# Performance work log

Hardware: AMD Instinct MI355X
Metric: run time of the kernel (lower is better)

## Reference

```python
import jax, jax.numpy as jnp
import numpy as np
import math

B, S, E = 32, 4096, 1024
H, D = 16, 64          # n_head, model_dim (per-head qk dim)
NV = E // H            # per-head value dim

def setup_inputs() -> dict:
    key = jax.random.key(0)
    ks = jax.random.split(key, 8)
    sc = 1.0 / math.sqrt(E)
    return {
        "seq1": jax.random.normal(ks[0], (B, 1, E), jnp.float32),
        "seq2": jax.random.normal(ks[1], (B, S, E), jnp.float32),
        "mask": jax.random.randint(ks[2], (B, 1, 1, S), 0, 2, jnp.int32),
        "Wq": jax.random.normal(ks[3], (E, H * D), jnp.float32) * sc,
        "bq": jnp.zeros((H * D,), jnp.float32),
        "Wk": jax.random.normal(ks[4], (E, H * D), jnp.float32) * sc,
        "bk": jnp.zeros((H * D,), jnp.float32),
        "Wv": jax.random.normal(ks[5], (E, E), jnp.float32) * sc,
        "bv": jnp.zeros((E,), jnp.float32),
    }

def reference(seq1, seq2, mask, Wq, bq, Wk, bk, Wv, bv):
    batch, seq_num, dim = seq2.shape
    q = seq1 @ Wq + bq                                   # [B,1,H*D]
    k = seq2 @ Wk + bk                                   # [B,S,H*D]
    v = seq2 @ Wv + bv                                   # [B,S,E]
    q = q.reshape(batch, 1, H, D).transpose(0, 2, 1, 3)      # [B,H,1,D]
    k = k.reshape(batch, seq_num, H, D).transpose(0, 2, 1, 3) # [B,H,S,D]
    v = v.reshape(batch, seq_num, H, NV).transpose(0, 2, 1, 3)# [B,H,S,NV]
    score = jnp.einsum('bhqd,bhkd->bhqk', q, k) / math.sqrt(D)  # [B,H,1,S]
    score = jnp.where(mask == 0, jnp.float32(-1e9), score)
    attn = jax.nn.softmax(score, axis=-1)
    out = jnp.einsum('bhqk,bhkn->bhqn', attn, v)             # [B,H,1,NV]
    return out.transpose(0, 2, 1, 3).reshape(batch, 1, dim)   # [B,1,E]
```

## Files before the change

kernel.cpp:

```cpp
#include <hip/hip_runtime.h>

#define B_  32
#define S_  4096
#define E_  1024
#define H_  16
#define D_  64
#define NV_ 64
#define HD_ 1024

typedef unsigned short ushort_t;
typedef __attribute__((ext_vector_type(8))) short  short8;
typedef __attribute__((ext_vector_type(4))) float  floatx4;

__device__ __forceinline__ ushort_t f2b(float f) {
  union { float f; unsigned int u; } v; v.f = f;
  return (ushort_t)((v.u + 0x7FFFu + ((v.u >> 16) & 1u)) >> 16);
}
__device__ __forceinline__ unsigned int pk2(float lo, float hi) {
  union { float f; unsigned int u; } a, b; a.f = lo; b.f = hi;
  return ((a.u + 0x8000u) >> 16) | ((b.u + 0x8000u) & 0xFFFF0000u);
}

__global__ __launch_bounds__(256) void qr_kernel(
    const float* __restrict__ seq1, const float* __restrict__ Wq,
    const float* __restrict__ bq,   const float* __restrict__ Wk,
    ushort_t* __restrict__ r_bf) {
  __shared__ __align__(16) float qp[4][64];
  __shared__ __align__(16) float qv[64];
  const int b = blockIdx.x / H_, h = blockIdx.x % H_;
  const int t = threadIdx.x;
  const int d = t & 63, quarter = t >> 6;

  {
    const float* s1 = seq1 + (size_t)b * E_;
    const float* wq = Wq + h * D_ + d;
    float sum = 0.f;
    const int e0 = quarter * 256;
    for (int e = e0; e < e0 + 256; ++e)
      sum += s1[e] * wq[(size_t)e * HD_];
    qp[quarter][d] = sum;
  }
  __syncthreads();
  if (t < 64) qv[t] = qp[0][t] + qp[1][t] + qp[2][t] + qp[3][t] + bq[h * D_ + t];
  __syncthreads();

  for (int i = 0; i < 4; ++i) {
    const int e = t + 256 * i;
    const float* wk = Wk + (size_t)e * HD_ + h * D_;
    float rs = 0.f;
#pragma unroll
    for (int g = 0; g < 16; ++g) {
      const float4 w4 = *(const float4*)(wk + g * 4);
      rs += w4.x * qv[g * 4 + 0] + w4.y * qv[g * 4 + 1] +
            w4.z * qv[g * 4 + 2] + w4.w * qv[g * 4 + 3];
    }
    r_bf[((size_t)b * H_ + h) * E_ + e] = f2b(rs * 0.125f);
  }
}

__global__ __launch_bounds__(256) void attn_kernel(
    const float* __restrict__ seq2, const int* __restrict__ mask,
    const ushort_t* __restrict__ r_bf, float* __restrict__ cpart,
    float* __restrict__ mlpart, int NC, int TPC) {
  __shared__ __align__(16) ushort_t rS[16][1032];
  __shared__ __align__(16) ushort_t xS[16][1032];
  __shared__ __align__(16) float scp[4][16][17];
  __shared__ __align__(16) float Pt[16][16];
  __shared__ __align__(16) float mS[16], lS[16], alphaS[16];

  const int b = blockIdx.y, chunk = blockIdx.x;
  const int t = threadIdx.x;
  const int lane = t & 63, w = t >> 6;
  const int s0 = chunk * (TPC * 16);
  const int e0 = t * 4;

  {
    const uint4* src = (const uint4*)(r_bf + (size_t)b * H_ * E_);
#pragma unroll
    for (int i = 0; i < 8; ++i) {
      const int f = t + 256 * i;
      *(uint4*)&rS[f >> 7][(f & 127) * 8] = src[f];
    }
  }
  if (t < 16) { mS[t] = -3e38f; lS[t] = 0.f; }

  float c[16][4];
#pragma unroll
  for (int h = 0; h < 16; ++h)
#pragma unroll
    for (int j = 0; j < 4; ++j) c[h][j] = 0.f;

  for (int it = 0; it < TPC; ++it) {
    const int st = s0 + it * 16;
    __syncthreads();
    {
      const float4* src = (const float4*)(seq2 + ((size_t)b * S_ + st) * E_);
#pragma unroll
      for (int i = 0; i < 16; ++i) {
        const int f = t + 256 * i;
        const float4 v = src[f];
        *(uint2*)&xS[f >> 8][(f & 255) * 4] =
            make_uint2(pk2(v.x, v.y), pk2(v.z, v.w));
      }
    }
    __syncthreads();

    {
      const int m = lane & 15, q = lane >> 4;
      floatx4 acc = {0.f, 0.f, 0.f, 0.f};
#pragma unroll
      for (int kk = 0; kk < 8; ++kk) {
        const int kb = w * 256 + kk * 32 + q * 8;
        short8 av  = *(const short8*)&xS[m][kb];
        short8 bvf = *(const short8*)&rS[m][kb];
        acc = __builtin_amdgcn_mfma_f32_16x16x32_bf16(av, bvf, acc, 0, 0, 0);
      }
#pragma unroll
      for (int j = 0; j < 4; ++j)
        scp[w][q * 4 + j][m] = acc[j];
    }
    __syncthreads();

    if (w == 0) {
      const int h = lane & 15, sg = lane >> 4;
      float sc[4];
#pragma unroll
      for (int j = 0; j < 4; ++j) {
        const int s = sg * 4 + j;
        float v = scp[0][s][h] + scp[1][s][h] + scp[2][s][h] + scp[3][s][h];
        if (mask[(size_t)b * S_ + st + s] == 0) v = -1e9f;
        sc[j] = v;
      }
      float tm = fmaxf(fmaxf(sc[0], sc[1]), fmaxf(sc[2], sc[3]));
      tm = fmaxf(tm, __shfl_xor(tm, 16));
      tm = fmaxf(tm, __shfl_xor(tm, 32));
      const float mo = mS[h];
      const float nm = fmaxf(mo, tm);
      const float al = __expf(mo - nm);
      float ps = 0.f;
#pragma unroll
      for (int j = 0; j < 4; ++j) {
        const float p = __expf(sc[j] - nm);
        Pt[sg * 4 + j][h] = p;
        ps += p;
      }
      ps += __shfl_xor(ps, 16);
      ps += __shfl_xor(ps, 32);
      if (lane < 16) { mS[h] = nm; alphaS[h] = al; lS[h] = lS[h] * al + ps; }
    }
    __syncthreads();

    {
#pragma unroll
      for (int h = 0; h < 16; ++h) {
        const float a = alphaS[h];
        c[h][0] *= a; c[h][1] *= a; c[h][2] *= a; c[h][3] *= a;
      }
#pragma unroll
      for (int s = 0; s < 16; ++s) {
        union { uint2 v; ushort_t u[4]; } xr;
        xr.v = *(const uint2*)&xS[s][e0];
        union { unsigned int i; float f; } cv;
        cv.i = (unsigned int)xr.u[0] << 16; const float x0 = cv.f;
        cv.i = (unsigned int)xr.u[1] << 16; const float x1 = cv.f;
        cv.i = (unsigned int)xr.u[2] << 16; const float x2 = cv.f;
        cv.i = (unsigned int)xr.u[3] << 16; const float x3 = cv.f;
        float p[16];
        *(float4*)&p[0]  = *(const float4*)&Pt[s][0];
        *(float4*)&p[4]  = *(const float4*)&Pt[s][4];
        *(float4*)&p[8]  = *(const float4*)&Pt[s][8];
        *(float4*)&p[12] = *(const float4*)&Pt[s][12];
#pragma unroll
        for (int h = 0; h < 16; ++h) {
          c[h][0] += p[h] * x0; c[h][1] += p[h] * x1;
          c[h][2] += p[h] * x2; c[h][3] += p[h] * x3;
        }
      }
    }
  }

  const size_t base = ((size_t)b * NC + chunk) * H_ * E_;
#pragma unroll
  for (int h = 0; h < 16; ++h)
    *(float4*)&cpart[base + (size_t)h * E_ + e0] =
        make_float4(c[h][0], c[h][1], c[h][2], c[h][3]);
  if (t < 16) {
    mlpart[(((size_t)b * NC + chunk) * H_ + t) * 2 + 0] = mS[t];
    mlpart[(((size_t)b * NC + chunk) * H_ + t) * 2 + 1] = lS[t];
  }
}

__global__ __launch_bounds__(256) void combine_kernel(
    const float* __restrict__ cpart, const float* __restrict__ mlpart,
    const float* __restrict__ Wv, const float* __restrict__ bvp,
    float* __restrict__ out, int NC) {
  __shared__ __align__(16) float wS[64];
  __shared__ __align__(16) float cnS[1024];
  __shared__ __align__(16) float vp[4][64];
  __shared__ float invLS;
  const int b = blockIdx.x / H_, h = blockIdx.x % H_;
  const int t = threadIdx.x;

  if (t < 64) {
    float m_i = -3e38f, l_i = 0.f;
    if (t < NC) {
      const size_t mi = (((size_t)b * NC + t) * H_ + h) * 2;
      m_i = mlpart[mi]; l_i = mlpart[mi + 1];
    }
    float M = m_i;
#pragma unroll
    for (int dlt = 1; dlt < 64; dlt <<= 1) M = fmaxf(M, __shfl_xor(M, dlt));
    const float wi = (t < NC) ? __expf(m_i - M) : 0.f;
    float Lp = l_i * wi;
#pragma unroll
    for (int dlt = 1; dlt < 64; dlt <<= 1) Lp += __shfl_xor(Lp, dlt);
    if (t < NC) wS[t] = wi;
    if (t == 0) invLS = 1.f / Lp;
  }
  __syncthreads();

  {
    const int e0 = t * 4;
    float a0 = 0.f, a1 = 0.f, a2 = 0.f, a3 = 0.f;
    for (int i = 0; i < NC; ++i) {
      const float wi = wS[i];
      const float4 v =
          *(const float4*)&cpart[(((size_t)b * NC + i) * H_ + h) * E_ + e0];
      a0 += wi * v.x; a1 += wi * v.y; a2 += wi * v.z; a3 += wi * v.w;
    }
    const float inv = invLS;
    *(float4*)&cnS[e0] = make_float4(a0 * inv, a1 * inv, a2 * inv, a3 * inv);
  }
  __syncthreads();

  {
    const int n = t & 63, part = t >> 6;
    const float* wv = Wv + h * NV_ + n;
    float sum = 0.f;
    const int eb = part * 256;
    for (int e = eb; e < eb + 256; ++e)
      sum += cnS[e] * wv[(size_t)e * E_];
    vp[part][n] = sum;
  }
  __syncthreads();
  if (t < 64) {
    const float o = vp[0][t] + vp[1][t] + vp[2][t] + vp[3][t] + bvp[h * NV_ + t];
    out[(size_t)b * E_ + h * NV_ + t] = o;
  }
}

extern "C" void kernel_launch(void* const* d_in, const int* in_sizes, int n_in,
                              void* d_out, int out_size, void* d_ws, size_t ws_size,
                              hipStream_t stream) {
  const float* seq1 = (const float*)d_in[0];
  const float* seq2 = (const float*)d_in[1];
  const int*   mask = (const int*)d_in[2];
  const float* Wq   = (const float*)d_in[3];
  const float* bq   = (const float*)d_in[4];
  const float* Wk   = (const float*)d_in[5];
  const float* Wv   = (const float*)d_in[7];
  const float* bv   = (const float*)d_in[8];
  float* out = (float*)d_out;

  const size_t rbytes = (size_t)B_ * H_ * E_ * 2;
  int NC = 16;
  while (NC > 1) {
    const size_t need = rbytes + (size_t)B_ * NC * H_ * E_ * 4
                               + (size_t)B_ * NC * H_ * 2 * 4;
    if (need <= ws_size) break;
    NC >>= 1;
  }
  const int TPC = (S_ / NC) / 16;
  ushort_t* r_bf = (ushort_t*)d_ws;
  float* cpart   = (float*)((char*)d_ws + rbytes);
  float* mlpart  = (float*)((char*)d_ws + rbytes + (size_t)B_ * NC * H_ * E_ * 4);

  qr_kernel<<<dim3(B_ * H_), dim3(256), 0, stream>>>(seq1, Wq, bq, Wk, r_bf);
  attn_kernel<<<dim3(NC, B_), dim3(256), 0, stream>>>(seq2, mask, r_bf, cpart,
                                                      mlpart, NC, TPC);
  combine_kernel<<<dim3(B_ * H_), dim3(256), 0, stream>>>(cpart, mlpart, Wv, bv,
                                                          out, NC);
}
```

Before: 796.1 us.

## Double-buffer seq2 tiles with register prefetch and keep softmax state in registers

The attention kernel now double-buffers the bf16 seq2 tile in LDS. The next tile's global loads are issued into registers before the current tile's MFMA work and written to the other buffer afterwards, which removes one barrier per iteration and hides load latency. The r vector is held in registers as MFMA operands, mask values are prefetched, and every wave computes the softmax redundantly with running max and sum in registers instead of wave 0 alone. Launch bounds request 2 blocks per CU, and unroll pragmas are added to the small GEMV loops. The costs are higher register pressure from 16 prefetched float4 values plus the accumulators, which may cause spills under the occupancy hint, and duplicated softmax work across waves.

Result: slower. 856.0 us (+7.5%).

```diff
diff --git a/kernel.cpp b/kernel.cpp
--- a/kernel.cpp
+++ b/kernel.cpp
@@ -19,6 +19,12 @@
 __device__ __forceinline__ unsigned int pk2(float lo, float hi) {
   union { float f; unsigned int u; } a, b; a.f = lo; b.f = hi;
   return ((a.u + 0x8000u) >> 16) | ((b.u + 0x8000u) & 0xFFFF0000u);
+}
+
+__device__ __forceinline__ void bar_lds() {
+  asm volatile("s_waitcnt lgkmcnt(0)" ::: "memory");
+  __builtin_amdgcn_s_barrier();
+  asm volatile("" ::: "memory");
 }
 
 __global__ __launch_bounds__(256) void qr_kernel(
@@ -36,6 +42,7 @@
     const float* wq = Wq + h * D_ + d;
     float sum = 0.f;
     const int e0 = quarter * 256;
+#pragma unroll 8
     for (int e = e0; e < e0 + 256; ++e)
       sum += s1[e] * wq[(size_t)e * HD_];
     qp[quarter][d] = sum;
@@ -58,97 +65,121 @@
   }
 }
 
-__global__ __launch_bounds__(256) void attn_kernel(
+__global__ __launch_bounds__(256, 2) void attn_kernel(
     const float* __restrict__ seq2, const int* __restrict__ mask,
     const ushort_t* __restrict__ r_bf, float* __restrict__ cpart,
     float* __restrict__ mlpart, int NC, int TPC) {
-  __shared__ __align__(16) ushort_t rS[16][1032];
-  __shared__ __align__(16) ushort_t xS[16][1032];
+  __shared__ __align__(16) ushort_t xbuf[2][16][1032];
   __shared__ __align__(16) float scp[4][16][17];
   __shared__ __align__(16) float Pt[16][16];
-  __shared__ __align__(16) float mS[16], lS[16], alphaS[16];
+  __shared__ __align__(16) float alphaS[16];
 
   const int b = blockIdx.y, chunk = blockIdx.x;
   const int t = threadIdx.x;
   const int lane = t & 63, w = t >> 6;
   const int s0 = chunk * (TPC * 16);
   const int e0 = t * 4;
-
+  const int m = lane & 15, q = lane >> 4;
+
+  const float4* xsrc = (const float4*)(seq2 + ((size_t)b * S_ + s0) * E_);
+  const int* mbase = mask + (size_t)b * S_ + s0 + q * 4;
+
+  uint4 rstage[8];
   {
     const uint4* src = (const uint4*)(r_bf + (size_t)b * H_ * E_);
 #pragma unroll
-    for (int i = 0; i < 8; ++i) {
-      const int f = t + 256 * i;
-      *(uint4*)&rS[f >> 7][(f & 127) * 8] = src[f];
-    }
-  }
-  if (t < 16) { mS[t] = -3e38f; lS[t] = 0.f; }
+    for (int i = 0; i < 8; ++i) rstage[i] = src[t + 256 * i];
+  }
+  int4 mk = *(const int4*)(mbase);
+  float4 v[16];
+#pragma unroll
+  for (int i = 0; i < 16; ++i) v[i] = xsrc[t + 256 * i];
+
+#pragma unroll
+  for (int i = 0; i < 8; ++i) {
+    const int f = t + 256 * i;
+    *(uint4*)&xbuf[1][f >> 7][(f & 127) * 8] = rstage[i];
+  }
+  bar_lds();
+  short8 rf[8];
+#pragma unroll
+  for (int kk = 0; kk < 8; ++kk)
+    rf[kk] = *(const short8*)&xbuf[1][m][w * 256 + kk * 32 + q * 8];
+  bar_lds();
+
+#pragma unroll
+  for (int i = 0; i < 16; ++i)
+    *(uint2*)&xbuf[0][i][e0] =
+        make_uint2(pk2(v[i].x, v[i].y), pk2(v[i].z, v[i].w));
+  bar_lds();
 
   float c[16][4];
 #pragma unroll
   for (int h = 0; h < 16; ++h)
 #pragma unroll
     for (int j = 0; j < 4; ++j) c[h][j] = 0.f;
+  float m_reg = -3e38f, l_reg = 0.f;
 
   for (int it = 0; it < TPC; ++it) {
-    const int st = s0 + it * 16;
-    __syncthreads();
+    const int cur = it & 1, nxt = cur ^ 1;
+    const bool pf = (it + 1 < TPC);
+    int4 mk_n;
+    if (pf) {
+      mk_n = *(const int4*)(mbase + (it + 1) * 16);
+#pragma unroll
+      for (int i = 0; i < 16; ++i)
+        v[i] = xsrc[(it + 1) * 4096 + t + 256 * i];
+    }
     {
-      const float4* src = (const float4*)(seq2 + ((size_t)b * S_ + st) * E_);
-#pragma unroll
-      for (int i = 0; i < 16; ++i) {
-        const int f = t + 256 * i;
-        const float4 v = src[f];
-        *(uint2*)&xS[f >> 8][(f & 255) * 4] =
-            make_uint2(pk2(v.x, v.y), pk2(v.z, v.w));
-      }
-    }
-    __syncthreads();
+      floatx4 acc = {0.f, 0.f, 0.f, 0.f};
+      __builtin_amdgcn_s_setprio(1);
+#pragma unroll
+      for (int kk = 0; kk < 8; ++kk) {
+        short8 av = *(const short8*)&xbuf[cur][m][w * 256 + kk * 32 + q * 8];
+        acc = __builtin_amdgcn_mfma_f32_16x16x32_bf16(av, rf[kk], acc, 0, 0, 0);
+      }
+      __builtin_amdgcn_s_setprio(0);
+#pragma unroll
+      for (int j = 0; j < 4; ++j) scp[w][q * 4 + j][m] = acc[j];
+    }
+    bar_lds();
 
     {
-      const int m = lane & 15, q = lane >> 4;
-      floatx4 acc = {0.f, 0.f, 0.f, 0.f};
-#pragma unroll
-      for (int kk = 0; kk < 8; ++kk) {
-        const int kb = w * 256 + kk * 32 + q * 8;
-        short8 av  = *(const short8*)&xS[m][kb];
-        short8 bvf = *(const short8*)&rS[m][kb];
-        acc = __builtin_amdgcn_mfma_f32_16x16x32_bf16(av, bvf, acc, 0, 0, 0);
-      }
-#pragma unroll
-      for (int j = 0; j < 4; ++j)
-        scp[w][q * 4 + j][m] = acc[j];
-    }
-    __syncthreads();
-
-    if (w == 0) {
-      const int h = lane & 15, sg = lane >> 4;
       float sc[4];
+      const int* mks = (const int*)&mk;
 #pragma unroll
       for (int j = 0; j < 4; ++j) {
-        const int s = sg * 4 + j;
-        float v = scp[0][s][h] + scp[1][s][h] + scp[2][s][h] + scp[3][s][h];
-        if (mask[(size_t)b * S_ + st + s] == 0) v = -1e9f;
-        sc[j] = v;
+        const int s = q * 4 + j;
+        float vv = scp[0][s][m] + scp[1][s][m] + scp[2][s][m] + scp[3][s][m];
+        if (mks[j] == 0) vv = -1e9f;
+        sc[j] = vv;
       }
       float tm = fmaxf(fmaxf(sc[0], sc[1]), fmaxf(sc[2], sc[3]));
       tm = fmaxf(tm, __shfl_xor(tm, 16));
       tm = fmaxf(tm, __shfl_xor(tm, 32));
-      const float mo = mS[h];
-      const float nm = fmaxf(mo, tm);
-      const float al = __expf(mo - nm);
-      float ps = 0.f;
-#pragma unroll
-      for (int j = 0; j < 4; ++j) {
-        const float p = __expf(sc[j] - nm);
-        Pt[sg * 4 + j][h] = p;
-        ps += p;
-      }
+      const float nm = fmaxf(m_reg, tm);
+      const float al = __expf(m_reg - nm);
+      const float p0 = __expf(sc[0] - nm), p1 = __expf(sc[1] - nm);
+      const float p2 = __expf(sc[2] - nm), p3 = __expf(sc[3] - nm);
+      if (q == w) {
+        Pt[q * 4 + 0][m] = p0; Pt[q * 4 + 1][m] = p1;
+        Pt[q * 4 + 2][m] = p2; Pt[q * 4 + 3][m] = p3;
+      }
+      float ps = (p0 + p1) + (p2 + p3);
       ps += __shfl_xor(ps, 16);
       ps += __shfl_xor(ps, 32);
-      if (lane < 16) { mS[h] = nm; alphaS[h] = al; lS[h] = lS[h] * al + ps; }
-    }
-    __syncthreads();
+      l_reg = l_reg * al + ps;
+      m_reg = nm;
+      if (t < 16) alphaS[t] = al;
+    }
+    if (pf) {
+#pragma unroll
+      for (int i = 0; i < 16; ++i)
+        *(uint2*)&xbuf[nxt][i][e0] =
+            make_uint2(pk2(v[i].x, v[i].y), pk2(v[i].z, v[i].w));
+      mk = mk_n;
+    }
+    bar_lds();
 
     {
 #pragma unroll
@@ -158,8 +189,8 @@
       }
 #pragma unroll
       for (int s = 0; s < 16; ++s) {
-        union { uint2 v; ushort_t u[4]; } xr;
-        xr.v = *(const uint2*)&xS[s][e0];
+        union { uint2 uv; ushort_t u[4]; } xr;
+        xr.uv = *(const uint2*)&xbuf[cur][s][e0];
         union { unsigned int i; float f; } cv;
         cv.i = (unsigned int)xr.u[0] << 16; const float x0 = cv.f;
         cv.i = (unsigned int)xr.u[1] << 16; const float x1 = cv.f;
@@ -185,8 +216,8 @@
     *(float4*)&cpart[base + (size_t)h * E_ + e0] =
         make_float4(c[h][0], c[h][1], c[h][2], c[h][3]);
   if (t < 16) {
-    mlpart[(((size_t)b * NC + chunk) * H_ + t) * 2 + 0] = mS[t];
-    mlpart[(((size_t)b * NC + chunk) * H_ + t) * 2 + 1] = lS[t];
+    mlpart[(((size_t)b * NC + chunk) * H_ + t) * 2 + 0] = m_reg;
+    mlpart[(((size_t)b * NC + chunk) * H_ + t) * 2 + 1] = l_reg;
   }
 }
 
@@ -238,6 +269,7 @@
     const float* wv = Wv + h * NV_ + n;
     float sum = 0.f;
     const int eb = part * 256;
+#pragma unroll 8
     for (int e = eb; e < eb + 256; ++e)
       sum += cnS[e] * wv[(size_t)e * E_];
     vp[part][n] = sum;
```
